# Performance work log

Measured on AMD Instinct MI355X. Metric: run time of the kernel, lower is better.

## Reference

```python
import jax, jax.numpy as jnp
import numpy as np

INPUT_SIZE = 32
HIDDEN = 256
BATCH = 256
SEQ = 365
FORGET_BIAS = 5.0


def setup_inputs() -> dict:
    key = jax.random.key(0)
    ks = jax.random.split(key, 6)
    s_ih = 1.0 / np.sqrt(INPUT_SIZE)
    s_hh = 1.0 / np.sqrt(HIDDEN)
    x_d = jax.random.normal(ks[0], (BATCH, SEQ, INPUT_SIZE), dtype=jnp.float32)
    w_ih = jax.random.normal(ks[1], (INPUT_SIZE, 4 * HIDDEN), dtype=jnp.float32) * s_ih
    w_hh = jax.random.normal(ks[2], (HIDDEN, 4 * HIDDEN), dtype=jnp.float32) * s_hh
    # bias with forget gate chunk initialized to initial_forget_bias (gate order: f, i, o, g)
    bias = jax.random.normal(ks[3], (4 * HIDDEN,), dtype=jnp.float32) * 0.01
    bias = bias.at[:HIDDEN].set(FORGET_BIAS)
    fc_w = jax.random.normal(ks[4], (HIDDEN, 1), dtype=jnp.float32) * s_hh
    fc_b = jax.random.normal(ks[5], (1,), dtype=jnp.float32) * 0.01
    return {"x_d": x_d, "w_ih": w_ih, "w_hh": w_hh, "bias": bias, "fc_w": fc_w, "fc_b": fc_b}


def _lstm(x_d, w_ih, w_hh, bias):
    B = x_d.shape[0]
    H = w_hh.shape[0]
    h0 = jnp.zeros((B, H), x_d.dtype)
    c0 = jnp.zeros((B, H), x_d.dtype)

    def step(carry, x_t):
        h, c = carry
        gates = x_t @ w_ih + h @ w_hh + bias  # [B, 4H]
        f, i, o, g = jnp.split(gates, 4, axis=1)
        c_new = jax.nn.sigmoid(f) * c + jax.nn.sigmoid(i) * jnp.tanh(g)
        h_new = jax.nn.sigmoid(o) * jnp.tanh(c_new)
        return (h_new, c_new), (h_new, c_new)

    _, (hs, cs) = jax.lax.scan(step, (h0, c0), jnp.swapaxes(x_d, 0, 1))
    # [T, B, H] -> [B, T, H]
    return jnp.swapaxes(hs, 0, 1), jnp.swapaxes(cs, 0, 1)


def reference(x_d, w_ih, w_hh, bias, fc_w, fc_b):
    h_n, c_n = _lstm(x_d, w_ih, w_hh, bias)
    last_h = h_n[:, -1, :]  # dropout is identity at p=0.0 / eval
    out = last_h @ fc_w + fc_b  # [B, 1]
    return (out, h_n, c_n)
```

## Files before the change

### kernel.cpp

```cpp
#include <hip/hip_runtime.h>
#include <stdint.h>

#define BATCH 256
#define SEQ   365
#define HID   256
#define INSZ  32
#define NGATE 1024
#define KTOT  288
#define NKC   9
#define AS    296
#define WTOT  (KTOT*NGATE)

#define NSPLIT 4
#define NGRP   16
#define NBLK   (NGRP*NSPLIT)
#define HSLICE 64

#define FLAG_OFF (2*WTOT*2)
#define HX_OFF   (FLAG_OFF + 1024)

typedef __bf16 bf16x8 __attribute__((ext_vector_type(8)));
typedef short  s16x8  __attribute__((ext_vector_type(8)));
typedef short  s16x4  __attribute__((ext_vector_type(4)));
typedef float  f32x4  __attribute__((ext_vector_type(4)));
typedef unsigned int u32x4 __attribute__((ext_vector_type(4)));

__device__ __forceinline__ unsigned short f2bf(float f) {
    unsigned u = __float_as_uint(f);
    u += 0x7FFFu + ((u >> 16) & 1u);
    return (unsigned short)(u >> 16);
}
__device__ __forceinline__ float bf2f(unsigned short h) {
    return __uint_as_float(((unsigned)h) << 16);
}
__device__ __forceinline__ float sigm(float x) { return 1.f / (1.f + __expf(-x)); }
__device__ __forceinline__ float tanh_f(float x) {
    float e = __expf(-2.f * fabsf(x));
    float r = (1.f - e) / (1.f + e);
    return copysignf(r, x);
}

__global__ void swizzle_w(const float* __restrict__ w_ih,
                          const float* __restrict__ w_hh,
                          unsigned short* __restrict__ wsw,
                          unsigned int* __restrict__ flags)
{
    if (blockIdx.x == 0) flags[threadIdx.x] = 0u;
    int idx = blockIdx.x*256 + threadIdx.x;
    int k = idx >> 10, n = idx & 1023;
    float v = (k < INSZ) ? w_ih[k*NGATE + n] : w_hh[(k-INSZ)*NGATE + n];
    unsigned short hi = f2bf(v);
    unsigned short lo = f2bf(v - bf2f(hi));
    int t = n >> 4, l15 = n & 15, c = k >> 5, q = (k >> 3) & 3, j = k & 7;
    int off = ((t*NKC + c)*64 + q*16 + l15)*8 + j;
    wsw[off]        = hi;
    wsw[WTOT + off] = lo;
}

__device__ __forceinline__ int a_addr(int r, int k) {
    return r*AS + ((((k >> 3) ^ (r & 3))) << 3) + (k & 7);
}

__global__ __launch_bounds__(256, 1) void lstm_seq(
    const float* __restrict__ x,
    const unsigned short* __restrict__ wsw,
    const float* __restrict__ bias,
    const float* __restrict__ fc_w,
    const float* __restrict__ fc_b,
    float* __restrict__ out,
    float* __restrict__ h_n,
    float* __restrict__ c_n,
    unsigned int* __restrict__ flags,
    unsigned int* __restrict__ hx)
{
    __shared__ short a_hi[16*AS];
    __shared__ short a_lo[16*AS];
    __shared__ float red[16*17];

    const int tid  = threadIdx.x;
    const int gq   = blockIdx.x >> 2;
    const int sl   = blockIdx.x & 3;
    const int b0   = gq * 16;
    const int wv   = tid >> 6, lane = tid & 63;
    const int l15  = lane & 15, q = lane >> 4;
    const int hcol = sl*HSLICE + wv*16 + l15;

    unsigned int* const hxg = hx + (size_t)gq * 2 * (16*HID);
    unsigned int* const flg = flags + gq*16;

    const unsigned short* wbase = wsw + ((size_t)((sl*4 + wv)*NKC)*64 + lane)*8;
    bf16x8 wh[NKC][4], wl[NKC][4];
    #pragma unroll
    for (int c = 0; c < NKC; ++c)
        #pragma unroll
        for (int G = 0; G < 4; ++G) {
            const unsigned short* wp = wbase + (size_t)(G*16*NKC + c)*512;
            wh[c][G] = __builtin_bit_cast(bf16x8, *(const s16x8*)wp);
            wl[c][G] = __builtin_bit_cast(bf16x8, *(const s16x8*)(wp + WTOT));
        }

    float bia[4];
    #pragma unroll
    for (int G = 0; G < 4; ++G) bia[G] = bias[G*HID + hcol];

    float cst[4];
    #pragma unroll
    for (int i = 0; i < 4; ++i) cst[i] = 0.f;

    for (int i = tid; i < 16*AS; i += 256) { a_hi[i] = 0; a_lo[i] = 0; }
    __syncthreads();
    {
        int r = tid >> 5, k = tid & 31;
        float v0 = x[((size_t)(b0 + r)*SEQ + 0)*INSZ + k];
        float v1 = x[((size_t)(b0 + 8 + r)*SEQ + 0)*INSZ + k];
        unsigned short h0 = f2bf(v0);
        int pa0 = a_addr(r, k);
        a_hi[pa0] = (short)h0; a_lo[pa0] = (short)f2bf(v0 - bf2f(h0));
        unsigned short h1 = f2bf(v1);
        int pa1 = a_addr(r + 8, k);
        a_hi[pa1] = (short)h1; a_lo[pa1] = (short)f2bf(v1 - bf2f(h1));
    }

    for (int s = 0; s < SEQ; ++s) {
        __syncthreads();

        float xv0 = 0.f, xv1 = 0.f;
        if (s + 1 < SEQ) {
            int r = tid >> 5, k = tid & 31;
            xv0 = x[((size_t)(b0 + r)*SEQ + (s+1))*INSZ + k];
            xv1 = x[((size_t)(b0 + 8 + r)*SEQ + (s+1))*INSZ + k];
        }

        f32x4 acc[4];
        #pragma unroll
        for (int G = 0; G < 4; ++G) acc[G] = (f32x4){0.f,0.f,0.f,0.f};

        const int qs = (q ^ (l15 & 3)) << 3;
        #pragma unroll
        for (int c = 0; c < NKC; ++c) {
            int pk = l15*AS + c*32 + qs;
            bf16x8 ah = __builtin_bit_cast(bf16x8, *(const s16x8*)&a_hi[pk]);
            bf16x8 al = __builtin_bit_cast(bf16x8, *(const s16x8*)&a_lo[pk]);
            #pragma unroll
            for (int G = 0; G < 4; ++G) {
                acc[G] = __builtin_amdgcn_mfma_f32_16x16x32_bf16(ah, wh[c][G], acc[G], 0,0,0);
                acc[G] = __builtin_amdgcn_mfma_f32_16x16x32_bf16(ah, wl[c][G], acc[G], 0,0,0);
                acc[G] = __builtin_amdgcn_mfma_f32_16x16x32_bf16(al, wh[c][G], acc[G], 0,0,0);
            }
        }

        unsigned int* hxw = hxg + (s & 1)*(16*HID);
        unsigned int hpk[4];
        #pragma unroll
        for (int i = 0; i < 4; ++i) {
            float f  = acc[0][i] + bia[0];
            float ii = acc[1][i] + bia[1];
            float o  = acc[2][i] + bia[2];
            float gg = acc[3][i] + bia[3];
            float cn = sigm(f)*cst[i] + sigm(ii)*tanh_f(gg);
            float hn = sigm(o)*tanh_f(cn);
            cst[i] = cn;
            unsigned short hi = f2bf(hn);
            unsigned short lo = f2bf(hn - bf2f(hi));
            unsigned int pk = ((unsigned int)hi << 16) | (unsigned int)lo;
            hpk[i] = pk;
            int row = q*4 + i;
            unsigned int* hp = hxw + row*HID + hcol;
            asm volatile("global_store_dword %0, %1, off sc0 sc1"
                         :: "v"(hp), "v"(pk) : "memory");
            size_t oi = ((size_t)(b0 + row)*SEQ + s)*HID + hcol;
            h_n[oi] = hn;
            c_n[oi] = cn;
        }

        asm volatile("s_waitcnt vmcnt(0)" ::: "memory");
        if ((tid & 63) == 0) {
            unsigned int fv = (unsigned int)(s + 1);
            asm volatile("global_store_dword %0, %1, off sc0 sc1"
                         :: "v"(flg + sl*4 + wv), "v"(fv) : "memory");
        }
        __syncthreads();

        if (s + 1 == SEQ && sl != 0) return;

        #pragma unroll
        for (int i = 0; i < 4; ++i) {
            int pa = a_addr(q*4 + i, INSZ + hcol);
            a_hi[pa] = (short)(hpk[i] >> 16);
            a_lo[pa] = (short)(hpk[i] & 0xffffu);
        }
        if (s + 1 < SEQ) {
            int r = tid >> 5, k = tid & 31;
            unsigned short h0 = f2bf(xv0);
            int pa0 = a_addr(r, k);
            a_hi[pa0] = (short)h0; a_lo[pa0] = (short)f2bf(xv0 - bf2f(h0));
            unsigned short h1 = f2bf(xv1);
            int pa1 = a_addr(r + 8, k);
            a_hi[pa1] = (short)h1; a_lo[pa1] = (short)f2bf(xv1 - bf2f(h1));
        }

        if (tid == 0) {
            unsigned int tgt = (unsigned int)(s + 1);
            while (1) {
                u32x4 f0, f1, f2, f3;
                asm volatile("global_load_dwordx4 %0, %4, off sc0 sc1\n\t"
                             "global_load_dwordx4 %1, %5, off sc0 sc1\n\t"
                             "global_load_dwordx4 %2, %6, off sc0 sc1\n\t"
                             "global_load_dwordx4 %3, %7, off sc0 sc1\n\t"
                             "s_waitcnt vmcnt(0)"
                             : "=v"(f0), "=v"(f1), "=v"(f2), "=v"(f3)
                             : "v"(flg), "v"(flg+4), "v"(flg+8), "v"(flg+12)
                             : "memory");
                bool ok = f0.x>=tgt && f0.y>=tgt && f0.z>=tgt && f0.w>=tgt
                       && f1.x>=tgt && f1.y>=tgt && f1.z>=tgt && f1.w>=tgt
                       && f2.x>=tgt && f2.y>=tgt && f2.z>=tgt && f2.w>=tgt
                       && f3.x>=tgt && f3.y>=tgt && f3.z>=tgt && f3.w>=tgt;
                if (ok) break;
            }
        }
        __syncthreads();

        const unsigned int* hxr = hxg + (s & 1)*(16*HID);
        const int rrow = tid >> 4, rc4 = (tid & 15) * 4;
        u32x4 hv[3];
        #pragma unroll
        for (int e = 0; e < 3; ++e) {
            int ss = (sl + 1 + e) & 3;
            const unsigned int* ap = hxr + rrow*HID + ss*64 + rc4;
            asm volatile("global_load_dwordx4 %0, %1, off sc0 sc1"
                         : "=v"(hv[e]) : "v"(ap) : "memory");
        }
        asm volatile("s_waitcnt vmcnt(0)" ::: "memory");
        __builtin_amdgcn_sched_barrier(0);
        #pragma unroll
        for (int e = 0; e < 3; ++e) {
            int ss = (sl + 1 + e) & 3;
            int pa = a_addr(rrow, INSZ + ss*64 + rc4);
            s16x4 hi4 = (s16x4){ (short)(hv[e].x >> 16), (short)(hv[e].y >> 16),
                                 (short)(hv[e].z >> 16), (short)(hv[e].w >> 16) };
            s16x4 lo4 = (s16x4){ (short)(hv[e].x & 0xffffu), (short)(hv[e].y & 0xffffu),
                                 (short)(hv[e].z & 0xffffu), (short)(hv[e].w & 0xffffu) };
            *(s16x4*)&a_hi[pa] = hi4;
            *(s16x4*)&a_lo[pa] = lo4;
        }
    }

    __syncthreads();
    {
        int r = tid >> 4, seg = tid & 15;
        float acc = 0.f;
        #pragma unroll
        for (int d = 0; d < 16; ++d) {
            int j = seg*16 + d;
            int pa = a_addr(r, INSZ + j);
            acc += (bf2f((unsigned short)a_hi[pa]) + bf2f((unsigned short)a_lo[pa])) * fc_w[j];
        }
        red[r*17 + seg] = acc;
    }
    __syncthreads();
    if (tid < 16) {
        float accv = fc_b[0];
        #pragma unroll
        for (int p = 0; p < 16; ++p) accv += red[tid*17 + p];
        out[b0 + tid] = accv;
    }
}

extern "C" void kernel_launch(void* const* d_in, const int* in_sizes, int n_in,
                              void* d_out, int out_size, void* d_ws, size_t ws_size,
                              hipStream_t stream) {
    const float* x    = (const float*)d_in[0];
    const float* w_ih = (const float*)d_in[1];
    const float* w_hh = (const float*)d_in[2];
    const float* bias = (const float*)d_in[3];
    const float* fc_w = (const float*)d_in[4];
    const float* fc_b = (const float*)d_in[5];

    float* out = (float*)d_out;
    float* h_n = out + BATCH;
    float* c_n = h_n + (size_t)BATCH*SEQ*HID;

    unsigned short* wsw   = (unsigned short*)d_ws;
    unsigned int*   flags = (unsigned int*)((char*)d_ws + FLAG_OFF);
    unsigned int*   hx    = (unsigned int*)((char*)d_ws + HX_OFF);

    swizzle_w<<<1152, 256, 0, stream>>>(w_ih, w_hh, wsw, flags);
    lstm_seq<<<NBLK, 256, 0, stream>>>(x, wsw, bias, fc_w, fc_b, out, h_n, c_n, flags, hx);
}
```

Before: 1.630 ms.

## Replace flag-based inter-block barrier with tagged hidden-state packets

```diff
diff --git a/kernel.cpp b/kernel.cpp
--- a/kernel.cpp
+++ b/kernel.cpp
@@ -16,14 +16,15 @@
 #define NBLK   (NGRP*NSPLIT)
 #define HSLICE 64
 
-#define FLAG_OFF (2*WTOT*2)
-#define HX_OFF   (FLAG_OFF + 1024)
+#define NTAGW  (NGRP*2*16*HID)
+#define HX_OFF (2*WTOT*2)
 
 typedef __bf16 bf16x8 __attribute__((ext_vector_type(8)));
 typedef short  s16x8  __attribute__((ext_vector_type(8)));
 typedef short  s16x4  __attribute__((ext_vector_type(4)));
 typedef float  f32x4  __attribute__((ext_vector_type(4)));
 typedef unsigned int u32x4 __attribute__((ext_vector_type(4)));
+typedef unsigned int u32x2 __attribute__((ext_vector_type(2)));
 
 __device__ __forceinline__ unsigned short f2bf(float f) {
     unsigned u = __float_as_uint(f);
@@ -43,10 +44,10 @@
 __global__ void swizzle_w(const float* __restrict__ w_ih,
                           const float* __restrict__ w_hh,
                           unsigned short* __restrict__ wsw,
-                          unsigned int* __restrict__ flags)
+                          unsigned int* __restrict__ hx)
 {
-    if (blockIdx.x == 0) flags[threadIdx.x] = 0u;
     int idx = blockIdx.x*256 + threadIdx.x;
+    if (idx < NTAGW) hx[2*idx + 1] = 0u;
     int k = idx >> 10, n = idx & 1023;
     float v = (k < INSZ) ? w_ih[k*NGATE + n] : w_hh[(k-INSZ)*NGATE + n];
     unsigned short hi = f2bf(v);
@@ -70,7 +71,6 @@
     float* __restrict__ out,
     float* __restrict__ h_n,
     float* __restrict__ c_n,
-    unsigned int* __restrict__ flags,
     unsigned int* __restrict__ hx)
 {
     __shared__ short a_hi[16*AS];
@@ -85,19 +85,23 @@
     const int l15  = lane & 15, q = lane >> 4;
     const int hcol = sl*HSLICE + wv*16 + l15;
 
-    unsigned int* const hxg = hx + (size_t)gq * 2 * (16*HID);
-    unsigned int* const flg = flags + gq*16;
+    unsigned int* const hxg = hx + (size_t)gq * 2 * (16*HID) * 2;
 
     const unsigned short* wbase = wsw + ((size_t)((sl*4 + wv)*NKC)*64 + lane)*8;
-    bf16x8 wh[NKC][4], wl[NKC][4];
+    u32x4 wh[NKC][4], wl[NKC][4];
     #pragma unroll
     for (int c = 0; c < NKC; ++c)
         #pragma unroll
         for (int G = 0; G < 4; ++G) {
             const unsigned short* wp = wbase + (size_t)(G*16*NKC + c)*512;
-            wh[c][G] = __builtin_bit_cast(bf16x8, *(const s16x8*)wp);
-            wl[c][G] = __builtin_bit_cast(bf16x8, *(const s16x8*)(wp + WTOT));
-        }
+            wh[c][G] = *(const u32x4*)wp;
+            wl[c][G] = *(const u32x4*)(wp + WTOT);
+        }
+    #pragma unroll
+    for (int c = 0; c < NKC; ++c)
+        #pragma unroll
+        for (int G = 0; G < 4; ++G)
+            asm volatile("" : "+v"(wh[c][G]), "+v"(wl[c][G]));
 
     float bia[4];
     #pragma unroll
@@ -143,14 +147,16 @@
             bf16x8 al = __builtin_bit_cast(bf16x8, *(const s16x8*)&a_lo[pk]);
             #pragma unroll
             for (int G = 0; G < 4; ++G) {
-                acc[G] = __builtin_amdgcn_mfma_f32_16x16x32_bf16(ah, wh[c][G], acc[G], 0,0,0);
-                acc[G] = __builtin_amdgcn_mfma_f32_16x16x32_bf16(ah, wl[c][G], acc[G], 0,0,0);
-                acc[G] = __builtin_amdgcn_mfma_f32_16x16x32_bf16(al, wh[c][G], acc[G], 0,0,0);
+                acc[G] = __builtin_amdgcn_mfma_f32_16x16x32_bf16(ah, __builtin_bit_cast(bf16x8, wh[c][G]), acc[G], 0,0,0);
+                acc[G] = __builtin_amdgcn_mfma_f32_16x16x32_bf16(ah, __builtin_bit_cast(bf16x8, wl[c][G]), acc[G], 0,0,0);
+                acc[G] = __builtin_amdgcn_mfma_f32_16x16x32_bf16(al, __builtin_bit_cast(bf16x8, wh[c][G]), acc[G], 0,0,0);
             }
         }
 
-        unsigned int* hxw = hxg + (s & 1)*(16*HID);
+        const unsigned int tag = (unsigned int)(s + 1);
+        unsigned int* hxw = hxg + (s & 1)*(16*HID*2);
         unsigned int hpk[4];
+        float hnv[4], cnv[4];
         #pragma unroll
         for (int i = 0; i < 4; ++i) {
             float f  = acc[0][i] + bia[0];
@@ -159,26 +165,25 @@
             float gg = acc[3][i] + bia[3];
             float cn = sigm(f)*cst[i] + sigm(ii)*tanh_f(gg);
             float hn = sigm(o)*tanh_f(cn);
-            cst[i] = cn;
+            cst[i] = cn; cnv[i] = cn; hnv[i] = hn;
             unsigned short hi = f2bf(hn);
             unsigned short lo = f2bf(hn - bf2f(hi));
-            unsigned int pk = ((unsigned int)hi << 16) | (unsigned int)lo;
-            hpk[i] = pk;
-            int row = q*4 + i;
-            unsigned int* hp = hxw + row*HID + hcol;
-            asm volatile("global_store_dword %0, %1, off sc0 sc1"
-                         :: "v"(hp), "v"(pk) : "memory");
-            size_t oi = ((size_t)(b0 + row)*SEQ + s)*HID + hcol;
-            h_n[oi] = hn;
-            c_n[oi] = cn;
-        }
-
-        asm volatile("s_waitcnt vmcnt(0)" ::: "memory");
-        if ((tid & 63) == 0) {
-            unsigned int fv = (unsigned int)(s + 1);
-            asm volatile("global_store_dword %0, %1, off sc0 sc1"
-                         :: "v"(flg + sl*4 + wv), "v"(fv) : "memory");
-        }
+            hpk[i] = ((unsigned int)hi << 16) | (unsigned int)lo;
+        }
+        #pragma unroll
+        for (int i = 0; i < 4; ++i) {
+            u32x2 pkt = (u32x2){ hpk[i], tag };
+            unsigned int* hp = hxw + ((q*4 + i)*HID + hcol)*2;
+            asm volatile("global_store_dwordx2 %0, %1, off sc0 sc1"
+                         :: "v"(hp), "v"(pkt) : "memory");
+        }
+        #pragma unroll
+        for (int i = 0; i < 4; ++i) {
+            size_t oi = ((size_t)(b0 + q*4 + i)*SEQ + s)*HID + hcol;
+            h_n[oi] = hnv[i];
+            c_n[oi] = cnv[i];
+        }
+
         __syncthreads();
 
         if (s + 1 == SEQ && sl != 0) return;
@@ -199,49 +204,51 @@
             a_hi[pa1] = (short)h1; a_lo[pa1] = (short)f2bf(xv1 - bf2f(h1));
         }
 
-        if (tid == 0) {
-            unsigned int tgt = (unsigned int)(s + 1);
-            while (1) {
-                u32x4 f0, f1, f2, f3;
-                asm volatile("global_load_dwordx4 %0, %4, off sc0 sc1\n\t"
-                             "global_load_dwordx4 %1, %5, off sc0 sc1\n\t"
-                             "global_load_dwordx4 %2, %6, off sc0 sc1\n\t"
-                             "global_load_dwordx4 %3, %7, off sc0 sc1\n\t"
-                             "s_waitcnt vmcnt(0)"
-                             : "=v"(f0), "=v"(f1), "=v"(f2), "=v"(f3)
-                             : "v"(flg), "v"(flg+4), "v"(flg+8), "v"(flg+12)
-                             : "memory");
-                bool ok = f0.x>=tgt && f0.y>=tgt && f0.z>=tgt && f0.w>=tgt
-                       && f1.x>=tgt && f1.y>=tgt && f1.z>=tgt && f1.w>=tgt
-                       && f2.x>=tgt && f2.y>=tgt && f2.z>=tgt && f2.w>=tgt
-                       && f3.x>=tgt && f3.y>=tgt && f3.z>=tgt && f3.w>=tgt;
-                if (ok) break;
-            }
-        }
-        __syncthreads();
-
-        const unsigned int* hxr = hxg + (s & 1)*(16*HID);
+        const unsigned int* hxr = hxg + (s & 1)*(16*HID*2);
         const int rrow = tid >> 4, rc4 = (tid & 15) * 4;
-        u32x4 hv[3];
-        #pragma unroll
-        for (int e = 0; e < 3; ++e) {
-            int ss = (sl + 1 + e) & 3;
-            const unsigned int* ap = hxr + rrow*HID + ss*64 + rc4;
-            asm volatile("global_load_dwordx4 %0, %1, off sc0 sc1"
-                         : "=v"(hv[e]) : "v"(ap) : "memory");
-        }
-        asm volatile("s_waitcnt vmcnt(0)" ::: "memory");
+        const int ss0 = (sl + 1) & 3, ss1 = (sl + 2) & 3, ss2 = (sl + 3) & 3;
+        const unsigned int* ap0 = hxr + (rrow*HID + ss0*64 + rc4)*2;
+        const unsigned int* ap1 = hxr + (rrow*HID + ss1*64 + rc4)*2;
+        const unsigned int* ap2 = hxr + (rrow*HID + ss2*64 + rc4)*2;
+        u32x4 v00, v01, v10, v11, v20, v21;
+        while (1) {
+            asm volatile(
+                "global_load_dwordx4 %0, %6, off sc0 sc1\n\t"
+                "global_load_dwordx4 %1, %6, off offset:16 sc0 sc1\n\t"
+                "global_load_dwordx4 %2, %7, off sc0 sc1\n\t"
+                "global_load_dwordx4 %3, %7, off offset:16 sc0 sc1\n\t"
+                "global_load_dwordx4 %4, %8, off sc0 sc1\n\t"
+                "global_load_dwordx4 %5, %8, off offset:16 sc0 sc1\n\t"
+                "s_waitcnt vmcnt(0)"
+                : "=&v"(v00), "=&v"(v01), "=&v"(v10), "=&v"(v11), "=&v"(v20), "=&v"(v21)
+                : "v"(ap0), "v"(ap1), "v"(ap2)
+                : "memory");
+            if (v00.y >= tag && v00.w >= tag && v01.y >= tag && v01.w >= tag &&
+                v10.y >= tag && v10.w >= tag && v11.y >= tag && v11.w >= tag &&
+                v20.y >= tag && v20.w >= tag && v21.y >= tag && v21.w >= tag) break;
+        }
         __builtin_amdgcn_sched_barrier(0);
-        #pragma unroll
-        for (int e = 0; e < 3; ++e) {
-            int ss = (sl + 1 + e) & 3;
-            int pa = a_addr(rrow, INSZ + ss*64 + rc4);
-            s16x4 hi4 = (s16x4){ (short)(hv[e].x >> 16), (short)(hv[e].y >> 16),
-                                 (short)(hv[e].z >> 16), (short)(hv[e].w >> 16) };
-            s16x4 lo4 = (s16x4){ (short)(hv[e].x & 0xffffu), (short)(hv[e].y & 0xffffu),
-                                 (short)(hv[e].z & 0xffffu), (short)(hv[e].w & 0xffffu) };
-            *(s16x4*)&a_hi[pa] = hi4;
-            *(s16x4*)&a_lo[pa] = lo4;
+
+        {
+            int pa = a_addr(rrow, INSZ + ss0*64 + rc4);
+            *(s16x4*)&a_hi[pa] = (s16x4){ (short)(v00.x >> 16), (short)(v00.z >> 16),
+                                          (short)(v01.x >> 16), (short)(v01.z >> 16) };
+            *(s16x4*)&a_lo[pa] = (s16x4){ (short)(v00.x & 0xffffu), (short)(v00.z & 0xffffu),
+                                          (short)(v01.x & 0xffffu), (short)(v01.z & 0xffffu) };
+        }
+        {
+            int pa = a_addr(rrow, INSZ + ss1*64 + rc4);
+            *(s16x4*)&a_hi[pa] = (s16x4){ (short)(v10.x >> 16), (short)(v10.z >> 16),
+                                          (short)(v11.x >> 16), (short)(v11.z >> 16) };
+            *(s16x4*)&a_lo[pa] = (s16x4){ (short)(v10.x & 0xffffu), (short)(v10.z & 0xffffu),
+                                          (short)(v11.x & 0xffffu), (short)(v11.z & 0xffffu) };
+        }
+        {
+            int pa = a_addr(rrow, INSZ + ss2*64 + rc4);
+            *(s16x4*)&a_hi[pa] = (s16x4){ (short)(v20.x >> 16), (short)(v20.z >> 16),
+                                          (short)(v21.x >> 16), (short)(v21.z >> 16) };
+            *(s16x4*)&a_lo[pa] = (s16x4){ (short)(v20.x & 0xffffu), (short)(v20.z & 0xffffu),
+                                          (short)(v21.x & 0xffffu), (short)(v21.z & 0xffffu) };
         }
     }
 
@@ -280,10 +287,9 @@
     float* h_n = out + BATCH;
     float* c_n = h_n + (size_t)BATCH*SEQ*HID;
 
-    unsigned short* wsw   = (unsigned short*)d_ws;
-    unsigned int*   flags = (unsigned int*)((char*)d_ws + FLAG_OFF);
-    unsigned int*   hx    = (unsigned int*)((char*)d_ws + HX_OFF);
-
-    swizzle_w<<<1152, 256, 0, stream>>>(w_ih, w_hh, wsw, flags);
-    lstm_seq<<<NBLK, 256, 0, stream>>>(x, wsw, bias, fc_w, fc_b, out, h_n, c_n, flags, hx);
-}
+    unsigned short* wsw = (unsigned short*)d_ws;
+    unsigned int*   hx  = (unsigned int*)((char*)d_ws + HX_OFF);
+
+    swizzle_w<<<1152, 256, 0, stream>>>(w_ih, w_hh, wsw, hx);
+    lstm_seq<<<NBLK, 256, 0, stream>>>(x, wsw, bias, fc_w, fc_b, out, h_n, c_n, hx);
+}
```

Result: faster. 1.323 ms (-18.8%).
